# Kernel tuning notes

Measured on AMD Instinct MI355X. Metric: run time of the kernel, lower is better.

The kernel has to match this reference:

```python
import jax, jax.numpy as jnp
from jax import lax
import numpy as np

LATENT = 512
LABEL = 128
BATCH = 1024


def _maxpool2(x):
    # 2x2 max pool, stride 2, NCHW
    return lax.reduce_window(x, -jnp.inf, lax.max, (1, 1, 2, 2), (1, 1, 2, 2), 'VALID')


def _encoder(x, c1w, c1b, c2w, c2b, fw, fb):
    dn = ('NCHW', 'OIHW', 'NCHW')
    y = lax.conv_general_dilated(x, c1w, (1, 1), 'SAME', dimension_numbers=dn)
    y = _maxpool2(jax.nn.relu(y + c1b[None, :, None, None]))  # [B,32,14,14]
    y = lax.conv_general_dilated(y, c2w, (1, 1), 'SAME', dimension_numbers=dn)
    y = _maxpool2(jax.nn.relu(y + c2b[None, :, None, None]))  # [B,64,7,7]
    y = y.reshape(y.shape[0], -1)                              # [B,3136]
    return y @ fw.T + fb                                       # [B,latent]


def _hopfield_w(rep):
    # rho = mean over ALL elements (matches torch.mean(x))
    rho = jnp.mean(rep)
    t = rep - rho                      # [label, latent]
    w = t.T @ t                        # sum of rank-1 outer products
    w = w * (1.0 - jnp.eye(w.shape[0], dtype=w.dtype))  # zero diagonal
    return w / LABEL


def _clustering(lat, w):
    # batched fixed-length Hopfield relaxation with min-energy tracking
    s0 = jnp.tanh(lat)                 # [B,L]
    B = s0.shape[0]

    def step(carry, _):
        s, min_e, min_s = carry
        prev = lax.stop_gradient(s)    # torch detaches prev_s each iter
        s_new = jnp.abs(prev) * jnp.sign(prev @ w.T)      # [B,L]
        e = -jnp.einsum('bi,ij,bj->b', s_new, w, s_new)    # [B]
        better = e < min_e
        min_e = jnp.where(better, e, min_e)
        min_s = jnp.where(better[:, None], s_new, min_s)
        return (s_new, min_e, min_s), None

    init = (s0, jnp.full((B,), jnp.inf, dtype=s0.dtype), jnp.zeros_like(s0))
    (_, _, min_s), _ = lax.scan(step, init, None, length=LATENT)
    return min_s


def setup_inputs() -> dict:
    key = jax.random.key(0)
    ks = jax.random.split(key, 11)
    d = {}
    d['image'] = jax.random.normal(ks[0], (BATCH, 1, 28, 28), dtype=jnp.float32)
    d['label_images'] = jax.random.uniform(ks[1], (LABEL, 1, 28, 28), dtype=jnp.float32)
    d['conv1_w'] = jax.random.normal(ks[2], (32, 1, 5, 5), dtype=jnp.float32) * 0.1
    d['conv1_b'] = jnp.zeros((32,), dtype=jnp.float32)
    d['conv2_w'] = jax.random.normal(ks[3], (64, 32, 5, 5), dtype=jnp.float32) * 0.05
    d['conv2_b'] = jnp.zeros((64,), dtype=jnp.float32)
    d['fc1_w'] = jax.random.normal(ks[4], (LATENT, 64 * 7 * 7), dtype=jnp.float32) * 0.02
    d['fc1_b'] = jnp.zeros((LATENT,), dtype=jnp.float32)
    d['fcn_w'] = jax.random.normal(ks[5], (LABEL, LATENT), dtype=jnp.float32) * 0.05
    d['fcn_b'] = jnp.zeros((LABEL,), dtype=jnp.float32)
    return d


def reference(image, label_images, conv1_w, conv1_b, conv2_w, conv2_b,
              fc1_w, fc1_b, fcn_w, fcn_b):
    rep = jnp.tanh(_encoder(label_images, conv1_w, conv1_b, conv2_w, conv2_b, fc1_w, fc1_b))  # [label,L]
    lat = _encoder(image, conv1_w, conv1_b, conv2_w, conv2_b, fc1_w, fc1_b)                    # [B,L]
    # FCN on detached latents (torch: .clone().detach())
    label = jax.nn.softmax(lax.stop_gradient(lat) @ fcn_w.T + fcn_b, axis=1)                   # [B,label]
    w = _hopfield_w(rep)                                                                        # [L,L]
    min_s = _clustering(lat, w)                                                                 # [B,L]
    out = jax.nn.softmax(jnp.abs(min_s @ rep.T), axis=1)                                        # [B,label]
    return (out, label)
```

## Files before the change

kernel.cpp:

```cpp
#include <hip/hip_runtime.h>
#include <hip/hip_bf16.h>
#include <math.h>

#define BATCH 1024
#define LABEL 128
#define LATENT 512
#define NTOT 1152

typedef short short8 __attribute__((ext_vector_type(8)));
typedef float f32x16 __attribute__((ext_vector_type(16)));

__device__ __forceinline__ unsigned short f2bf(float f) {
    __hip_bfloat16 h = __float2bfloat16(f);
    return *(unsigned short*)&h;
}
__device__ __forceinline__ float bf2f(unsigned short u) {
    __hip_bfloat16 h; *(unsigned short*)&h = u;
    return __bfloat162float(h);
}

#define BSTR ((size_t)512 * 3136)
#define ASTR ((size_t)NTOT * 3136)
#define A2STR ((size_t)BATCH * 512)
#define W2STR ((size_t)LABEL * 512)


__global__ __launch_bounds__(256) void conv1_pool(const float* __restrict__ image,
                                                  const float* __restrict__ limg,
                                                  const float* __restrict__ wt,
                                                  const float* __restrict__ bias,
                                                  unsigned short* __restrict__ o1b) {
    const int n = blockIdx.x;
    const float* in = (n < BATCH) ? (image + (size_t)n * 784)
                                  : (limg + (size_t)(n - BATCH) * 784);
    __shared__ float pin[32][32];
    __shared__ float wts[32 * 25];
    const int tid = threadIdx.x;
    unsigned short* ob = o1b + (size_t)n * 12800;
    for (int i = tid; i < 256; i += 256) {
        int pl_ = i >> 7, r = i & 127;
        ob[pl_ * 6400 + 6272 + r] = 0;
    }
    for (int idx = tid; idx < 32 * 32; idx += 256) ((float*)pin)[idx] = 0.f;
    __syncthreads();
    for (int idx = tid; idx < 784; idx += 256) {
        int y = idx / 28, x = idx % 28;
        pin[y + 2][x + 2] = in[idx];
    }
    for (int idx = tid; idx < 800; idx += 256) wts[idx] = wt[idx];
    __syncthreads();
    const int oc = tid & 31;
    float wk[25];
    #pragma unroll
    for (int k = 0; k < 25; ++k) wk[k] = wts[oc * 25 + k];
    const float b = bias[oc];
    const int slot_lo = (oc & 7);
    const int gq = oc >> 3;
    for (int it = 0; it < 2; ++it) {
        const int py = (tid >> 5) + it * 8;
        if (py >= 14) continue;
        #pragma unroll
        for (int xh = 0; xh < 2; ++xh) {
            const int acol = xh ? 12 : 0;
            const int off = xh ? 2 : 0;
            float a0[14], a1[14];
            #pragma unroll
            for (int c = 0; c < 14; ++c) { a0[c] = b; a1[c] = b; }
            #pragma unroll
            for (int t = 0; t < 6; ++t) {
                float row[20];
                const float4* rp = (const float4*)&pin[2 * py + t][acol];
                #pragma unroll
                for (int v = 0; v < 5; ++v) {
                    float4 f = rp[v];
                    row[4 * v] = f.x; row[4 * v + 1] = f.y;
                    row[4 * v + 2] = f.z; row[4 * v + 3] = f.w;
                }
                if (t < 5) {
                    #pragma unroll
                    for (int kx = 0; kx < 5; ++kx) {
                        float w0 = wk[t * 5 + kx];
                        #pragma unroll
                        for (int c = 0; c < 14; ++c)
                            a0[c] = fmaf(row[c + kx + off], w0, a0[c]);
                    }
                }
                if (t >= 1) {
                    #pragma unroll
                    for (int kx = 0; kx < 5; ++kx) {
                        float w1 = wk[(t - 1) * 5 + kx];
                        #pragma unroll
                        for (int c = 0; c < 14; ++c)
                            a1[c] = fmaf(row[c + kx + off], w1, a1[c]);
                    }
                }
            }
            #pragma unroll
            for (int px = 0; px < 7; ++px) {
                float v = fmaxf(fmaxf(a0[2 * px], a0[2 * px + 1]),
                                fmaxf(a1[2 * px], a1[2 * px + 1]));
                v = fmaxf(v, 0.f);
                unsigned short b1 = f2bf(v);
                unsigned short b2 = f2bf(v - bf2f(b1));
                int p = py * 14 + 7 * xh + px;
                int offo = p * 32 + (((gq ^ (p >> 1)) & 3) << 3) + slot_lo;
                ob[offo] = b1; ob[6400 + offo] = b2;
            }
        }
    }
}

__global__ __launch_bounds__(256) void prep(const float* __restrict__ c2w,
                                            const float* __restrict__ f1w,
                                            const float* __restrict__ fnw,
                                            unsigned short* __restrict__ Bf,
                                            unsigned short* __restrict__ Bw2,
                                            unsigned short* __restrict__ Bn2) {
    int idx = blockIdx.x * 256 + threadIdx.x;
    if (idx < 102400) {
        int j = idx & 7, lane = (idx >> 3) & 63, ocT = (idx >> 9) & 1, s = idx >> 10;
        int q = lane >> 5, nn = lane & 31;
        int k = 16 * s + 8 * q + j;
        int tap = k >> 5, ic = k & 31;
        int oc = 32 * ocT + nn;
        float v = c2w[oc * 800 + ic * 25 + tap];
        unsigned short b1 = f2bf(v);
        unsigned short b2 = f2bf(v - bf2f(b1));
        size_t base = ((size_t)(s * 2 + ocT) * 2) * 512 + lane * 8 + j;
        Bf[base] = b1; Bf[base + 512] = b2;
        return;
    }
    int i2 = idx - 102400;
    if (i2 < 512 * 3136) {
        float v = f1w[i2];
        unsigned short b1 = f2bf(v);
        unsigned short b2 = f2bf(v - bf2f(b1));
        Bw2[i2] = b1; Bw2[BSTR + i2] = b2;
        return;
    }
    int i3 = i2 - 512 * 3136;
    if (i3 >= 128 * 512) return;
    float v = fnw[i3];
    unsigned short b1 = f2bf(v);
    unsigned short b2 = f2bf(v - bf2f(b1));
    Bn2[i3] = b1; Bn2[W2STR + i3] = b2;
}

template<int NT>
__device__ __forceinline__ void conv2_kloop(const unsigned short* __restrict__ pl,
                                            const unsigned short* __restrict__ Bf,
                                            const int ocT, const int lane, const int q,
                                            const int* __restrict__ ym,
                                            const int* __restrict__ xm,
                                            const int* __restrict__ mm,
                                            f32x16* __restrict__ acc) {
    for (int s = 0; s < 50; ++s) {
        const unsigned short* bp = Bf + ((size_t)(s * 2 + ocT) * 2) * 512 + lane * 8;
        short8 b1 = *(const short8*)(bp);
        short8 b2 = *(const short8*)(bp + 512);
        int kb = 16 * s + 8 * q;
        int tap = kb >> 5, ic0 = kb & 31, g = ic0 >> 3;
        int ky = (tap * 13) >> 6;
        int kx = tap - ky * 5;
        int iyk = ky - 2, ixk = kx - 2;
        int pq2 = iyk * 14 + ixk;
        short8 a1[NT], a2[NT];
        #pragma unroll
        for (int tt = 0; tt < NT; ++tt) {
            int iy = ym[tt] + iyk, ix = xm[tt] + ixk;
            int valid = ((unsigned)iy < 14u) & ((unsigned)ix < 14u);
            int cpt = valid ? (mm[tt] + pq2) : 196;
            int addr = cpt * 32 + (((g ^ (cpt >> 1)) & 3) << 3);
            a1[tt] = *(const short8*)(pl + addr);
            a2[tt] = *(const short8*)(pl + 6400 + addr);
        }
        #pragma unroll
        for (int tt = 0; tt < NT; ++tt)
            acc[tt] = __builtin_amdgcn_mfma_f32_32x32x16_bf16(a1[tt], b1, acc[tt], 0, 0, 0);
        #pragma unroll
        for (int tt = 0; tt < NT; ++tt)
            acc[tt] = __builtin_amdgcn_mfma_f32_32x32x16_bf16(a1[tt], b2, acc[tt], 0, 0, 0);
        #pragma unroll
        for (int tt = 0; tt < NT; ++tt)
            acc[tt] = __builtin_amdgcn_mfma_f32_32x32x16_bf16(a2[tt], b1, acc[tt], 0, 0, 0);
    }
}

__global__ __launch_bounds__(256) void conv2_mfma(const unsigned short* __restrict__ o1b,
                                                  const unsigned short* __restrict__ Bf,
                                                  const float* __restrict__ bias,
                                                  unsigned short* __restrict__ out2) {
    const int n = blockIdx.x;
    __shared__ __align__(16) unsigned short pl[12800];
    const int tid = threadIdx.x;
    const int lane = tid & 63, wv = tid >> 6;
    const int ocT = wv & 1, mh = wv >> 1;

    {
        const float4* src = (const float4*)(o1b + (size_t)n * 12800);
        float4* dst = (float4*)pl;
        for (int i = tid; i < 1600; i += 256) dst[i] = src[i];
    }
    __syncthreads();

    const int m_ = lane & 31, q = lane >> 5;
    int ym[4], xm[4], mm[4];
    #pragma unroll
    for (int tt = 0; tt < 4; ++tt) {
        int t = 4 * mh + tt;
        if (t > 6) t = 6;
        int m = 32 * t + m_;
        mm[tt] = m;
        ym[tt] = m / 14;
        xm[tt] = m - 14 * ym[tt];
    }
    f32x16 acc[4];
    {
        float bs = bias[32 * ocT + m_];
        #pragma unroll
        for (int tt = 0; tt < 4; ++tt)
        #pragma unroll
        for (int r = 0; r < 16; ++r) acc[tt][r] = bs;
    }

    if (mh == 0) conv2_kloop<4>(pl, Bf, ocT, lane, q, ym, xm, mm, acc);
    else         conv2_kloop<3>(pl, Bf, ocT, lane, q, ym, xm, mm, acc);
    __syncthreads();

    float* hx = (float*)pl;
    {
        const int oc = 32 * ocT + m_;
        #pragma unroll
        for (int tt = 0; tt < 4; ++tt)
        #pragma unroll
        for (int e = 0; e < 8; ++e) {
            const int reg = 2 * e;
            const int r = (reg & 3) + 8 * (reg >> 2) + 4 * q;
            const int m = 32 * (4 * mh + tt) + r;
            if (m < 196) {
                float xm2 = fmaxf(acc[tt][reg], acc[tt][reg + 1]);
                int y = (m * 2341) >> 15;
                int px = (m - 14 * y) >> 1;
                hx[(y * 7 + px) * 65 + oc] = xm2;
            }
        }
    }
    __syncthreads();

    for (int idx = tid; idx < 3136; idx += 256) {
        int oc2 = (idx * 2675) >> 17;
        int p = idx - 49 * oc2;
        int py = (p * 9363) >> 16;
        int px = p - 7 * py;
        float v = fmaxf(hx[(2 * py * 7 + px) * 65 + oc2],
                        hx[((2 * py + 1) * 7 + px) * 65 + oc2]);
        v = fmaxf(v, 0.f);
        unsigned short b1 = f2bf(v);
        unsigned short b2 = f2bf(v - bf2f(b1));
        size_t o = (size_t)n * 3136 + idx;
        out2[o] = b1; out2[ASTR + o] = b2;
    }
}

__global__ __launch_bounds__(256) void fc1_mfma(const unsigned short* __restrict__ A2,
                                                const unsigned short* __restrict__ B2,
                                                float* __restrict__ part) {
    __shared__ unsigned short As[2][2048];
    __shared__ unsigned short Bs[2][2048];
    const int tid = threadIdx.x;
    const int n0 = blockIdx.x * 64, m0 = blockIdx.y * 64;
    const int koff = blockIdx.z * 448;
    const int lr = tid >> 2, g = tid & 3;
    const int slot = (((g ^ (lr >> 1)) & 3) << 3);
    const int lane = tid & 63, wv = tid >> 6;
    const int nq = wv & 1, mq = wv >> 1;
    const int q = lane >> 5, l31 = lane & 31;
    const int rA = 32 * nq + l31, rB = 32 * mq + l31;
    f32x16 acc;
    #pragma unroll
    for (int r = 0; r < 16; ++r) acc[r] = 0.f;

    for (int bk = 0; bk < 448; bk += 32) {
        const size_t ka = (size_t)(koff + bk + (g << 3));
        short8 av[2], bv[2];
        #pragma unroll
        for (int p = 0; p < 2; ++p) {
            av[p] = *(const short8*)(A2 + p * ASTR + (size_t)(n0 + lr) * 3136 + ka);
            bv[p] = *(const short8*)(B2 + p * BSTR + (size_t)(m0 + lr) * 3136 + ka);
        }
        __syncthreads();
        #pragma unroll
        for (int p = 0; p < 2; ++p) {
            *(short8*)&As[p][(lr << 5) + slot] = av[p];
            *(short8*)&Bs[p][(lr << 5) + slot] = bv[p];
        }
        __syncthreads();
        #pragma unroll
        for (int s2 = 0; s2 < 32; s2 += 16) {
            const int gg = (s2 + (q << 3)) >> 3;
            const int sa = (((gg ^ (rA >> 1)) & 3) << 3);
            const int sb = (((gg ^ (rB >> 1)) & 3) << 3);
            short8 a1 = *(const short8*)&As[0][(rA << 5) + sa];
            short8 a2 = *(const short8*)&As[1][(rA << 5) + sa];
            short8 b1 = *(const short8*)&Bs[0][(rB << 5) + sb];
            short8 b2 = *(const short8*)&Bs[1][(rB << 5) + sb];
            acc = __builtin_amdgcn_mfma_f32_32x32x16_bf16(a1, b1, acc, 0, 0, 0);
            acc = __builtin_amdgcn_mfma_f32_32x32x16_bf16(a1, b2, acc, 0, 0, 0);
            acc = __builtin_amdgcn_mfma_f32_32x32x16_bf16(a2, b1, acc, 0, 0, 0);
        }
    }
    float* pb = part + (size_t)blockIdx.z * NTOT * 512;
    #pragma unroll
    for (int reg = 0; reg < 16; ++reg) {
        int nn = n0 + 32 * nq + (reg & 3) + 8 * (reg >> 2) + 4 * q;
        int mmo = m0 + 32 * mq + l31;
        pb[(size_t)nn * 512 + mmo] = acc[reg];
    }
}

__global__ __launch_bounds__(256) void fc1_reduce(const float* __restrict__ part,
                                                  const float* __restrict__ bias,
                                                  float* __restrict__ lat,
                                                  unsigned short* __restrict__ lat2,
                                                  float* __restrict__ rep) {
    int idx = blockIdx.x * 256 + threadIdx.x;
    int m = idx & 511;
    float v = bias[m];
    #pragma unroll
    for (int kz = 0; kz < 7; ++kz) v += part[(size_t)kz * NTOT * 512 + idx];
    if (idx < BATCH * 512) {
        lat[idx] = v;
        unsigned short b1 = f2bf(v);
        lat2[idx] = b1;
        lat2[A2STR + idx] = f2bf(v - bf2f(b1));
    } else {
        rep[idx - BATCH * 512] = tanhf(v);
    }
}

__global__ __launch_bounds__(256) void fcn_mfma(const unsigned short* __restrict__ A2,
                                                const unsigned short* __restrict__ B2,
                                                float* __restrict__ logits) {
    __shared__ unsigned short As[2][2048];
    __shared__ unsigned short Bs[2][2048];
    const int tid = threadIdx.x;
    const int n0 = blockIdx.x * 64, m0 = blockIdx.y * 64;
    const int lr = tid >> 2, g = tid & 3;
    const int slot = (((g ^ (lr >> 1)) & 3) << 3);
    const int lane = tid & 63, wv = tid >> 6;
    const int nq = wv & 1, mq = wv >> 1;
    const int q = lane >> 5, l31 = lane & 31;
    const int rA = 32 * nq + l31, rB = 32 * mq + l31;
    f32x16 acc;
    #pragma unroll
    for (int r = 0; r < 16; ++r) acc[r] = 0.f;

    for (int bk = 0; bk < 512; bk += 32) {
        const size_t ka = (size_t)(bk + (g << 3));
        short8 av[2], bv[2];
        #pragma unroll
        for (int p = 0; p < 2; ++p) {
            av[p] = *(const short8*)(A2 + p * A2STR + (size_t)(n0 + lr) * 512 + ka);
            bv[p] = *(const short8*)(B2 + p * W2STR + (size_t)(m0 + lr) * 512 + ka);
        }
        __syncthreads();
        #pragma unroll
        for (int p = 0; p < 2; ++p) {
            *(short8*)&As[p][(lr << 5) + slot] = av[p];
            *(short8*)&Bs[p][(lr << 5) + slot] = bv[p];
        }
        __syncthreads();
        #pragma unroll
        for (int s2 = 0; s2 < 32; s2 += 16) {
            const int gg = (s2 + (q << 3)) >> 3;
            const int sa = (((gg ^ (rA >> 1)) & 3) << 3);
            const int sb = (((gg ^ (rB >> 1)) & 3) << 3);
            short8 a1 = *(const short8*)&As[0][(rA << 5) + sa];
            short8 a2 = *(const short8*)&As[1][(rA << 5) + sa];
            short8 b1 = *(const short8*)&Bs[0][(rB << 5) + sb];
            short8 b2 = *(const short8*)&Bs[1][(rB << 5) + sb];
            acc = __builtin_amdgcn_mfma_f32_32x32x16_bf16(a1, b1, acc, 0, 0, 0);
            acc = __builtin_amdgcn_mfma_f32_32x32x16_bf16(a1, b2, acc, 0, 0, 0);
            acc = __builtin_amdgcn_mfma_f32_32x32x16_bf16(a2, b1, acc, 0, 0, 0);
        }
    }
    #pragma unroll
    for (int reg = 0; reg < 16; ++reg) {
        int nn = n0 + 32 * nq + (reg & 3) + 8 * (reg >> 2) + 4 * q;
        int mmo = m0 + 32 * mq + l31;
        logits[(size_t)nn * 128 + mmo] = acc[reg];
    }
}

__global__ __launch_bounds__(128) void fcn_softmax2(const float* __restrict__ logits,
                                                    const float* __restrict__ fb,
                                                    float* __restrict__ out) {
    const int b = blockIdx.x;
    const int j = threadIdx.x;
    __shared__ float red[128];
    float acc = logits[(size_t)b * 128 + j] + fb[j];
    red[j] = acc;
    __syncthreads();
    for (int off = 64; off >= 1; off >>= 1) {
        if (j < off) red[j] = fmaxf(red[j], red[j + off]);
        __syncthreads();
    }
    float mx = red[0];
    __syncthreads();
    float ex = expf(acc - mx);
    red[j] = ex;
    __syncthreads();
    for (int off = 64; off >= 1; off >>= 1) {
        if (j < off) red[j] += red[j + off];
        __syncthreads();
    }
    out[(size_t)b * 128 + j] = ex / red[0];
}

__global__ __launch_bounds__(256) void rho_kernel(const float* __restrict__ rep,
                                                  float* __restrict__ rho) {
    __shared__ float red[256];
    const int tid = threadIdx.x;
    float s = 0.f;
    for (int i = tid; i < LABEL * LATENT; i += 256) s += rep[i];
    red[tid] = s;
    __syncthreads();
    for (int off = 128; off >= 1; off >>= 1) {
        if (tid < off) red[tid] += red[tid + off];
        __syncthreads();
    }
    if (tid == 0) rho[0] = red[0] / (float)(LABEL * LATENT);
}

__global__ __launch_bounds__(256) void t_kernel(const float* __restrict__ rep,
                                                const float* __restrict__ rho,
                                                float* __restrict__ tT) {
    __shared__ float tile[64][65];
    const int tid = threadIdx.x;
    const int i0 = blockIdx.x * 64, k0 = blockIdx.y * 64;
    const int tx = tid & 63, ty4 = tid >> 6;
    const float r0 = rho[0];
    #pragma unroll
    for (int rr = 0; rr < 16; ++rr) {
        int kk = ty4 * 16 + rr;
        tile[kk][tx] = rep[(size_t)(k0 + kk) * 512 + i0 + tx];
    }
    __syncthreads();
    #pragma unroll
    for (int rr = 0; rr < 16; ++rr) {
        int ii = ty4 * 16 + rr;
        tT[(size_t)(i0 + ii) * 128 + k0 + tx] = tile[tx][ii] - r0;
    }
}

__global__ __launch_bounds__(256) void w_kernel(const float* __restrict__ tT,
                                                float* __restrict__ w) {
    int idx = blockIdx.x * 256 + threadIdx.x;
    int i = idx >> 9, j = idx & 511;
    const float4* a = (const float4*)(tT + i * 128);
    const float4* b = (const float4*)(tT + j * 128);
    float acc = 0.f;
    #pragma unroll 8
    for (int q = 0; q < 32; ++q) {
        float4 av = a[q], bv = b[q];
        acc += av.x * bv.x + av.y * bv.y + av.z * bv.z + av.w * bv.w;
    }
    w[idx] = (i == j) ? 0.f : acc * (1.f / 128.f);
}

__global__ __launch_bounds__(256) void hinit(const float* __restrict__ lat,
                                             const float* __restrict__ w,
                                             float* __restrict__ hmat) {
    __shared__ float As[16][68];
    __shared__ float Bs[16][68];
    const int tid = threadIdx.x;
    const int n0 = blockIdx.x * 64, m0 = blockIdx.y * 64;
    const int lr = tid >> 2;
    const int lk = (tid & 3) * 4;
    const int ty = tid >> 4, tx = tid & 15;
    float c[4][4] = {};
    for (int k0 = 0; k0 < 512; k0 += 16) {
        float4 a4 = *(const float4*)(lat + (size_t)(n0 + lr) * 512 + k0 + lk);
        float4 b4 = *(const float4*)(w + (size_t)(m0 + lr) * 512 + k0 + lk);
        a4.x = tanhf(a4.x); a4.y = tanhf(a4.y); a4.z = tanhf(a4.z); a4.w = tanhf(a4.w);
        __syncthreads();
        As[lk + 0][lr] = a4.x; As[lk + 1][lr] = a4.y; As[lk + 2][lr] = a4.z; As[lk + 3][lr] = a4.w;
        Bs[lk + 0][lr] = b4.x; Bs[lk + 1][lr] = b4.y; Bs[lk + 2][lr] = b4.z; Bs[lk + 3][lr] = b4.w;
        __syncthreads();
        #pragma unroll
        for (int kk = 0; kk < 16; ++kk) {
            float av[4], bv[4];
            #pragma unroll
            for (int i = 0; i < 4; ++i) av[i] = As[kk][ty * 4 + i];
            #pragma unroll
            for (int j = 0; j < 4; ++j) bv[j] = Bs[kk][tx * 4 + j];
            #pragma unroll
            for (int i = 0; i < 4; ++i)
            #pragma unroll
            for (int j = 0; j < 4; ++j) c[i][j] += av[i] * bv[j];
        }
    }
    #pragma unroll
    for (int i = 0; i < 4; ++i)
    #pragma unroll
    for (int j = 0; j < 4; ++j)
        hmat[(size_t)(n0 + ty * 4 + i) * 512 + m0 + tx * 4 + j] = c[i][j];
}

__device__ __forceinline__ float sgnf(float x) {
    return (x > 0.f) ? 1.f : ((x < 0.f) ? -1.f : 0.f);
}

__global__ __launch_bounds__(256) void clustering(const float* __restrict__ lat,
                                                  const float* __restrict__ hmat,
                                                  const float* __restrict__ w,
                                                  const float* __restrict__ rep,
                                                  float* __restrict__ out) {
    const int tid = threadIdx.x;
    const int row = blockIdx.x;
    __shared__ float mins[512];
    __shared__ float red[256];
    __shared__ float part_e[4];
    __shared__ int part_c[4];
    __shared__ float min_e_s;
    __shared__ int copyf_s;
    __shared__ int donef_s;
    __shared__ int cnt_s;
    __shared__ int jidx[512];
    __shared__ float jdel[512];
    const int i0 = 2 * tid, i1 = 2 * tid + 1;
    const int wave = tid >> 6, lane = tid & 63;

    float sm10, sm11, sm20, sm21, h0, h1;
    {
        sm10 = tanhf(lat[(size_t)row * 512 + i0]);
        sm11 = tanhf(lat[(size_t)row * 512 + i1]);
        sm20 = sm10; sm21 = sm11;
        h0 = hmat[(size_t)row * 512 + i0];
        h1 = hmat[(size_t)row * 512 + i1];
    }
    if (tid == 0) { min_e_s = INFINITY; donef_s = 0; cnt_s = 0; }
    __syncthreads();

    for (int k = 1; k <= 512; ++k) {
        float sn0 = fabsf(sm10) * sgnf(h0);
        float sn1 = fabsf(sm11) * sgnf(h1);
        int cy = (sn0 == sm20 && sn1 == sm21) ? 1 : 0;
        if (sn0 != sm10) {
            int p = atomicAdd(&cnt_s, 1);
            jidx[p] = i0; jdel[p] = sn0 - sm10;
        }
        if (sn1 != sm11) {
            int p = atomicAdd(&cnt_s, 1);
            jidx[p] = i1; jdel[p] = sn1 - sm11;
        }
        #pragma unroll
        for (int m = 32; m >= 1; m >>= 1) cy &= __shfl_xor(cy, m, 64);
        if (lane == 0) part_c[wave] = cy;
        __syncthreads();

        {
            const int c = cnt_s;
            #pragma unroll 8
            for (int t = 0; t < c; ++t) {
                const int j = jidx[t];
                const float d = jdel[t];
                const float2 wvv = *(const float2*)(w + (size_t)j * 512 + i0);
                h0 = fmaf(d, wvv.x, h0);
                h1 = fmaf(d, wvv.y, h1);
            }
        }
        float ep = sn0 * h0 + sn1 * h1;
        #pragma unroll
        for (int m = 32; m >= 1; m >>= 1) ep += __shfl_xor(ep, m, 64);
        if (lane == 0) part_e[wave] = ep;
        __syncthreads();

        if (tid == 0) {
            float e = -(part_e[0] + part_e[1] + part_e[2] + part_e[3]);
            int better = e < min_e_s;
            if (better) min_e_s = e;
            copyf_s = better;
            int fl = part_c[0] & part_c[1] & part_c[2] & part_c[3];
            int fixedp = (cnt_s == 0);
            int cyc = (k >= 2) && fl;
            if (fixedp || cyc) donef_s = 1;
            cnt_s = 0;
        }
        __syncthreads();

        if (copyf_s) { mins[i0] = sn0; mins[i1] = sn1; }
        sm20 = sm10; sm21 = sm11;
        sm10 = sn0;  sm11 = sn1;
        if (donef_s) break;
    }
    __syncthreads();

    const int j = tid & 127, half = tid >> 7;
    {
        const float4* rr = (const float4*)(rep + (size_t)j * 512 + half * 256);
        const float4* ms = (const float4*)(&mins[half * 256]);
        float p = 0.f;
        #pragma unroll 8
        for (int q = 0; q < 64; ++q) {
            float4 rv = rr[q], mv = ms[q];
            p += rv.x * mv.x + rv.y * mv.y + rv.z * mv.z + rv.w * mv.w;
        }
        red[tid] = p;
        __syncthreads();
        float v = 0.f;
        if (tid < 128) { v = fabsf(red[tid] + red[tid + 128]); red[tid] = v; }
        __syncthreads();
        for (int off = 64; off >= 1; off >>= 1) {
            if (tid < off) red[tid] = fmaxf(red[tid], red[tid + off]);
            __syncthreads();
        }
        float mx = red[0];
        __syncthreads();
        float ex = 0.f;
        if (tid < 128) { ex = expf(v - mx); red[tid] = ex; }
        __syncthreads();
        for (int off = 64; off >= 1; off >>= 1) {
            if (tid < off) red[tid] += red[tid + off];
            __syncthreads();
        }
        if (tid < 128) out[(size_t)row * 128 + tid] = ex / red[0];
    }
}

extern "C" void kernel_launch(void* const* d_in, const int* in_sizes, int n_in,
                              void* d_out, int out_size, void* d_ws, size_t ws_size,
                              hipStream_t stream) {
    const float* image = (const float*)d_in[0];
    const float* limg  = (const float*)d_in[1];
    const float* c1w   = (const float*)d_in[2];
    const float* c1b   = (const float*)d_in[3];
    const float* c2w   = (const float*)d_in[4];
    const float* c2b   = (const float*)d_in[5];
    const float* f1w   = (const float*)d_in[6];
    const float* f1b   = (const float*)d_in[7];
    const float* fnw   = (const float*)d_in[8];
    const float* fnb   = (const float*)d_in[9];
    float* out = (float*)d_out;
    float* ws  = (float*)d_ws;

    unsigned short* o1b  = (unsigned short*)ws;
    unsigned short* out2 = o1b + (size_t)NTOT * 12800;
    float* lat  = (float*)(out2 + 2 * ASTR);
    float* rep  = lat + (size_t)BATCH * 512;
    float* tT   = rep + (size_t)LABEL * 512;
    float* wmat = tT + (size_t)512 * 128;
    float* rho  = wmat + (size_t)512 * 512;
    unsigned short* Bw2   = (unsigned short*)(rho + 16);
    unsigned short* Bfrag = Bw2 + 2 * BSTR;
    float* hmat = (float*)(Bfrag + 102400);
    unsigned short* lat2 = (unsigned short*)(hmat + A2STR);
    unsigned short* fnw2 = lat2 + 2 * A2STR;
    float* logits = (float*)(fnw2 + 2 * W2STR);
    float* part = (float*)ws;

    const int prep_total = 102400 + 512 * 3136 + 128 * 512;
    hipLaunchKernelGGL(prep, dim3((prep_total + 255) / 256), dim3(256), 0, stream,
                       c2w, f1w, fnw, Bfrag, Bw2, fnw2);
    hipLaunchKernelGGL(conv1_pool, dim3(NTOT), dim3(256), 0, stream, image, limg, c1w, c1b, o1b);
    hipLaunchKernelGGL(conv2_mfma, dim3(NTOT), dim3(256), 0, stream, o1b, Bfrag, c2b, out2);
    hipLaunchKernelGGL(fc1_mfma, dim3(NTOT / 64, 512 / 64, 7), dim3(256), 0, stream,
                       out2, Bw2, part);
    hipLaunchKernelGGL(fc1_reduce, dim3(NTOT * 512 / 256), dim3(256), 0, stream,
                       part, f1b, lat, lat2, rep);
    hipLaunchKernelGGL(fcn_mfma, dim3(16, 2), dim3(256), 0, stream, lat2, fnw2, logits);
    hipLaunchKernelGGL(fcn_softmax2, dim3(BATCH), dim3(128), 0, stream, logits, fnb,
                       out + (size_t)BATCH * LABEL);
    hipLaunchKernelGGL(rho_kernel, dim3(1), dim3(256), 0, stream, rep, rho);
    hipLaunchKernelGGL(t_kernel, dim3(8, 2), dim3(256), 0, stream, rep, rho, tT);
    hipLaunchKernelGGL(w_kernel, dim3(1024), dim3(256), 0, stream, tT, wmat);
    hipLaunchKernelGGL(hinit, dim3(BATCH / 64, 512 / 64), dim3(256), 0, stream, lat, wmat, hmat);
    hipLaunchKernelGGL(clustering, dim3(BATCH), dim3(256), 0, stream,
                       lat, hmat, wmat, rep, out);
}
```

Before: 395.6 us.

## Process two images per conv2 block to reuse weight fragments across images

The conv2 MFMA kernel now handles two images per workgroup. Each wave covers both output-channel halves and fewer spatial tiles, so every loaded B fragment is reused across two images and two channel tiles. This cuts global weight loads per image and halves the grid size. In exchange it doubles LDS use, raises accumulator register pressure (8 f32x16 accumulators, with launch bounds asking for 2 blocks), and reduces the number of blocks available to fill the GPU.

```diff
diff --git a/kernel.cpp b/kernel.cpp
--- a/kernel.cpp
+++ b/kernel.cpp
@@ -147,117 +147,153 @@
 }
 
 template<int NT>
-__device__ __forceinline__ void conv2_kloop(const unsigned short* __restrict__ pl,
-                                            const unsigned short* __restrict__ Bf,
-                                            const int ocT, const int lane, const int q,
-                                            const int* __restrict__ ym,
-                                            const int* __restrict__ xm,
-                                            const int* __restrict__ mm,
-                                            f32x16* __restrict__ acc) {
+__device__ __forceinline__ void conv2_kloop2(const unsigned short* __restrict__ pl,
+                                             const unsigned short* __restrict__ Bf,
+                                             const int lane, const int q,
+                                             const int* __restrict__ ym,
+                                             const int* __restrict__ xm,
+                                             const int* __restrict__ mm,
+                                             const float bs0, const float bs1,
+                                             f32x16* __restrict__ acc) {
+    #pragma unroll
+    for (int im = 0; im < 2; ++im)
+    #pragma unroll
+    for (int oc = 0; oc < 2; ++oc) {
+        const float bs = oc ? bs1 : bs0;
+        #pragma unroll
+        for (int tt = 0; tt < NT; ++tt)
+        #pragma unroll
+        for (int r = 0; r < 16; ++r) acc[(im * 2 + oc) * NT + tt][r] = bs;
+    }
     for (int s = 0; s < 50; ++s) {
-        const unsigned short* bp = Bf + ((size_t)(s * 2 + ocT) * 2) * 512 + lane * 8;
-        short8 b1 = *(const short8*)(bp);
-        short8 b2 = *(const short8*)(bp + 512);
-        int kb = 16 * s + 8 * q;
-        int tap = kb >> 5, ic0 = kb & 31, g = ic0 >> 3;
-        int ky = (tap * 13) >> 6;
-        int kx = tap - ky * 5;
-        int iyk = ky - 2, ixk = kx - 2;
-        int pq2 = iyk * 14 + ixk;
-        short8 a1[NT], a2[NT];
+        const unsigned short* bp = Bf + (size_t)s * 2048 + lane * 8;
+        short8 b1[2], b2[2];
+        b1[0] = *(const short8*)(bp);
+        b2[0] = *(const short8*)(bp + 512);
+        b1[1] = *(const short8*)(bp + 1024);
+        b2[1] = *(const short8*)(bp + 1536);
+        const int kb = 16 * s + 8 * q;
+        const int tap = kb >> 5, g = (kb & 31) >> 3;
+        const int ky = (tap * 13) >> 6;
+        const int kx = tap - ky * 5;
+        const int iyk = ky - 2, ixk = kx - 2;
+        const int pq2 = iyk * 14 + ixk;
+        int addr[NT];
         #pragma unroll
         for (int tt = 0; tt < NT; ++tt) {
             int iy = ym[tt] + iyk, ix = xm[tt] + ixk;
             int valid = ((unsigned)iy < 14u) & ((unsigned)ix < 14u);
             int cpt = valid ? (mm[tt] + pq2) : 196;
-            int addr = cpt * 32 + (((g ^ (cpt >> 1)) & 3) << 3);
-            a1[tt] = *(const short8*)(pl + addr);
-            a2[tt] = *(const short8*)(pl + 6400 + addr);
-        }
-        #pragma unroll
-        for (int tt = 0; tt < NT; ++tt)
-            acc[tt] = __builtin_amdgcn_mfma_f32_32x32x16_bf16(a1[tt], b1, acc[tt], 0, 0, 0);
-        #pragma unroll
-        for (int tt = 0; tt < NT; ++tt)
-            acc[tt] = __builtin_amdgcn_mfma_f32_32x32x16_bf16(a1[tt], b2, acc[tt], 0, 0, 0);
-        #pragma unroll
-        for (int tt = 0; tt < NT; ++tt)
-            acc[tt] = __builtin_amdgcn_mfma_f32_32x32x16_bf16(a2[tt], b1, acc[tt], 0, 0, 0);
-    }
-}
-
-__global__ __launch_bounds__(256) void conv2_mfma(const unsigned short* __restrict__ o1b,
-                                                  const unsigned short* __restrict__ Bf,
-                                                  const float* __restrict__ bias,
-                                                  unsigned short* __restrict__ out2) {
-    const int n = blockIdx.x;
-    __shared__ __align__(16) unsigned short pl[12800];
+            addr[tt] = cpt * 32 + (((g ^ (cpt >> 1)) & 3) << 3);
+        }
+        short8 a1[2][NT], a2[2][NT];
+        #pragma unroll
+        for (int im = 0; im < 2; ++im) {
+            const unsigned short* pli = pl + im * 12800;
+            #pragma unroll
+            for (int tt = 0; tt < NT; ++tt) {
+                a1[im][tt] = *(const short8*)(pli + addr[tt]);
+                a2[im][tt] = *(const short8*)(pli + 6400 + addr[tt]);
+            }
+        }
+        #pragma unroll
+        for (int im = 0; im < 2; ++im)
+        #pragma unroll
+        for (int oc = 0; oc < 2; ++oc)
+        #pragma unroll
+        for (int tt = 0; tt < NT; ++tt) {
+            f32x16 a = acc[(im * 2 + oc) * NT + tt];
+            a = __builtin_amdgcn_mfma_f32_32x32x16_bf16(a1[im][tt], b1[oc], a, 0, 0, 0);
+            a = __builtin_amdgcn_mfma_f32_32x32x16_bf16(a1[im][tt], b2[oc], a, 0, 0, 0);
+            a = __builtin_amdgcn_mfma_f32_32x32x16_bf16(a2[im][tt], b1[oc], a, 0, 0, 0);
+            acc[(im * 2 + oc) * NT + tt] = a;
+        }
+    }
+}
+
+template<int NT>
+__device__ __forceinline__ void conv2_epi(const f32x16* __restrict__ acc,
+                                          float* __restrict__ hx,
+                                          const int wv, const int m_, const int q) {
+    #pragma unroll
+    for (int im = 0; im < 2; ++im) {
+        float* hxi = hx + im * 6400;
+        #pragma unroll
+        for (int oc = 0; oc < 2; ++oc) {
+            const int occ = 32 * oc + m_;
+            #pragma unroll
+            for (int tt = 0; tt < NT; ++tt)
+            #pragma unroll
+            for (int e = 0; e < 8; ++e) {
+                const int reg = 2 * e;
+                const int r = (reg & 3) + 8 * (reg >> 2) + 4 * q;
+                const int m = 32 * (2 * wv + tt) + r;
+                if (m < 196) {
+                    float xm2 = fmaxf(acc[(im * 2 + oc) * NT + tt][reg],
+                                      acc[(im * 2 + oc) * NT + tt][reg + 1]);
+                    int y = (m * 2341) >> 15;
+                    int px = (m - 14 * y) >> 1;
+                    hxi[(y * 7 + px) * 65 + occ] = xm2;
+                }
+            }
+        }
+    }
+}
+
+__global__ __launch_bounds__(256, 2) void conv2_mfma(const unsigned short* __restrict__ o1b,
+                                                     const unsigned short* __restrict__ Bf,
+                                                     const float* __restrict__ bias,
+                                                     unsigned short* __restrict__ out2) {
+    const int n2 = blockIdx.x;
+    __shared__ __align__(16) unsigned short pl[2 * 12800];
     const int tid = threadIdx.x;
     const int lane = tid & 63, wv = tid >> 6;
-    const int ocT = wv & 1, mh = wv >> 1;
 
     {
-        const float4* src = (const float4*)(o1b + (size_t)n * 12800);
+        const float4* src = (const float4*)(o1b + (size_t)n2 * 25600);
         float4* dst = (float4*)pl;
-        for (int i = tid; i < 1600; i += 256) dst[i] = src[i];
+        for (int i = tid; i < 3200; i += 256) dst[i] = src[i];
     }
     __syncthreads();
 
     const int m_ = lane & 31, q = lane >> 5;
-    int ym[4], xm[4], mm[4];
-    #pragma unroll
-    for (int tt = 0; tt < 4; ++tt) {
-        int t = 4 * mh + tt;
+    int ym[2], xm[2], mm[2];
+    #pragma unroll
+    for (int tt = 0; tt < 2; ++tt) {
+        int t = 2 * wv + tt;
         if (t > 6) t = 6;
         int m = 32 * t + m_;
         mm[tt] = m;
         ym[tt] = m / 14;
         xm[tt] = m - 14 * ym[tt];
     }
-    f32x16 acc[4];
-    {
-        float bs = bias[32 * ocT + m_];
-        #pragma unroll
-        for (int tt = 0; tt < 4; ++tt)
-        #pragma unroll
-        for (int r = 0; r < 16; ++r) acc[tt][r] = bs;
-    }
-
-    if (mh == 0) conv2_kloop<4>(pl, Bf, ocT, lane, q, ym, xm, mm, acc);
-    else         conv2_kloop<3>(pl, Bf, ocT, lane, q, ym, xm, mm, acc);
+    const float bs0 = bias[m_];
+    const float bs1 = bias[32 + m_];
+    f32x16 acc[8];
+
+    if (wv < 3) conv2_kloop2<2>(pl, Bf, lane, q, ym, xm, mm, bs0, bs1, acc);
+    else        conv2_kloop2<1>(pl, Bf, lane, q, ym, xm, mm, bs0, bs1, acc);
     __syncthreads();
 
     float* hx = (float*)pl;
-    {
-        const int oc = 32 * ocT + m_;
-        #pragma unroll
-        for (int tt = 0; tt < 4; ++tt)
-        #pragma unroll
-        for (int e = 0; e < 8; ++e) {
-            const int reg = 2 * e;
-            const int r = (reg & 3) + 8 * (reg >> 2) + 4 * q;
-            const int m = 32 * (4 * mh + tt) + r;
-            if (m < 196) {
-                float xm2 = fmaxf(acc[tt][reg], acc[tt][reg + 1]);
-                int y = (m * 2341) >> 15;
-                int px = (m - 14 * y) >> 1;
-                hx[(y * 7 + px) * 65 + oc] = xm2;
-            }
-        }
-    }
-    __syncthreads();
-
-    for (int idx = tid; idx < 3136; idx += 256) {
+    if (wv < 3) conv2_epi<2>(acc, hx, wv, m_, q);
+    else        conv2_epi<1>(acc, hx, wv, m_, q);
+    __syncthreads();
+
+    for (int ii = tid; ii < 6272; ii += 256) {
+        const int im = (ii >= 3136) ? 1 : 0;
+        const int idx = ii - (im ? 3136 : 0);
+        const float* hxi = hx + im * 6400;
         int oc2 = (idx * 2675) >> 17;
         int p = idx - 49 * oc2;
         int py = (p * 9363) >> 16;
         int px = p - 7 * py;
-        float v = fmaxf(hx[(2 * py * 7 + px) * 65 + oc2],
-                        hx[((2 * py + 1) * 7 + px) * 65 + oc2]);
+        float v = fmaxf(hxi[(2 * py * 7 + px) * 65 + oc2],
+                        hxi[((2 * py + 1) * 7 + px) * 65 + oc2]);
         v = fmaxf(v, 0.f);
         unsigned short b1 = f2bf(v);
         unsigned short b2 = f2bf(v - bf2f(b1));
-        size_t o = (size_t)n * 3136 + idx;
+        size_t o = (size_t)n2 * 6272 + ii;
         out2[o] = b1; out2[ASTR + o] = b2;
     }
 }
@@ -663,7 +699,7 @@
     hipLaunchKernelGGL(prep, dim3((prep_total + 255) / 256), dim3(256), 0, stream,
                        c2w, f1w, fnw, Bfrag, Bw2, fnw2);
     hipLaunchKernelGGL(conv1_pool, dim3(NTOT), dim3(256), 0, stream, image, limg, c1w, c1b, o1b);
-    hipLaunchKernelGGL(conv2_mfma, dim3(NTOT), dim3(256), 0, stream, o1b, Bfrag, c2b, out2);
+    hipLaunchKernelGGL(conv2_mfma, dim3(NTOT / 2), dim3(256), 0, stream, o1b, Bfrag, c2b, out2);
     hipLaunchKernelGGL(fc1_mfma, dim3(NTOT / 64, 512 / 64, 7), dim3(256), 0, stream,
                        out2, Bw2, part);
     hipLaunchKernelGGL(fc1_reduce, dim3(NTOT * 512 / 256), dim3(256), 0, stream,
```

Measured after the change: 390.1 us. No clear change (-1.4%).
